# Optimization experiments

Measured on AMD Instinct MI355X. Metric: run time of the kernel, lower is better.

Reference implementation:

```python
import jax, jax.numpy as jnp
import numpy as np

B, L, E, H = 1, 2048, 1024, 16
D = E // H
SCALE_BASE = 512.0
LN_EPS = 1e-5


def _rotate_every_two(x):
    x1 = x[..., ::2]
    x2 = x[..., 1::2]
    return jnp.stack((-x2, x1), axis=-1).reshape(x.shape)


def _xpos(x, downscale):
    # x: [B, H, L, D]; offset=0 path of torchscale XPOS
    length, dim = x.shape[-2], x.shape[-1]
    half = dim // 2
    base_scale = (jnp.arange(0, dim, 2, dtype=jnp.float32) + 0.4 * dim) / (1.4 * dim)  # [half]
    min_pos = -(length // 2)
    pos = jnp.arange(min_pos, min_pos + length, dtype=jnp.float32)  # [L]
    scale = base_scale[None, :] ** (pos[:, None] / SCALE_BASE)  # [L, half]
    inv_freq = 1.0 / (10000.0 ** (jnp.arange(half, dtype=jnp.float32) / half))
    sinusoid = jnp.arange(length, dtype=jnp.float32)[:, None] * inv_freq[None, :]  # [L, half]
    sin, cos = jnp.sin(sinusoid), jnp.cos(sinusoid)
    if downscale:
        scale = 1.0 / scale
    sin_s = jnp.repeat(sin * scale, 2, axis=-1)  # duplicate_interleave -> [L, D]
    cos_s = jnp.repeat(cos * scale, 2, axis=-1)
    return x * cos_s + _rotate_every_two(x) * sin_s


def setup_inputs() -> dict:
    key = jax.random.key(0)
    ks = jax.random.split(key, 8)
    s = 1.0 / np.sqrt(E)
    causal = jnp.where(jnp.triu(jnp.ones((L, L), dtype=bool), 1), -1e9, 0.0).astype(jnp.float32)
    return {
        "query": jax.random.normal(ks[0], (B, L, E), jnp.float32),
        "rel_pos": jax.random.normal(ks[1], (B * H, L, L), jnp.float32) * 0.02,
        "attn_mask": causal,
        "wq": jax.random.normal(ks[2], (E, E), jnp.float32) * s,
        "bq": jnp.zeros((E,), jnp.float32),
        "wk": jax.random.normal(ks[3], (E, E), jnp.float32) * s,
        "bk": jnp.zeros((E,), jnp.float32),
        "wv": jax.random.normal(ks[4], (E, E), jnp.float32) * s,
        "bv": jnp.zeros((E,), jnp.float32),
        "wo": jax.random.normal(ks[5], (E, E), jnp.float32) * s,
        "bo": jnp.zeros((E,), jnp.float32),
        "ln_g": jnp.ones((E,), jnp.float32),
        "ln_b": jnp.zeros((E,), jnp.float32),
    }


def reference(query, rel_pos, attn_mask, wq, bq, wk, bk, wv, bv, wo, bo, ln_g, ln_b):
    b, l, e = query.shape
    # QKV projections (self-attention: key=value=query)
    def split_heads(x):
        return x.reshape(b, l, H, D).transpose(0, 2, 1, 3)  # [B,H,L,D]
    q = split_heads(query @ wq.T + bq)
    k = split_heads(query @ wk.T + bk)
    v = split_heads(query @ wv.T + bv)
    # xpos rotary: keys downscaled, queries upscaled (offset=0, prefill)
    k = _xpos(k, downscale=True)
    q = _xpos(q, downscale=False)
    # scaled dot-product attention with additive causal mask + rel_pos bias
    q = q * (D ** -0.5)
    aw = jnp.einsum("bhtd,bhsd->bhts", q, k)
    aw = aw + attn_mask[None, None, :, :]
    aw = aw + rel_pos.reshape(b, H, l, l)
    aw = jax.nn.softmax(aw.astype(jnp.float32), axis=-1).astype(q.dtype)
    attn = jnp.einsum("bhts,bhsd->bhtd", aw, v)
    attn = attn.transpose(0, 2, 1, 3).reshape(b, l, e)  # [B, L, E]
    # inner_attn_ln (subln)
    mu = jnp.mean(attn, axis=-1, keepdims=True)
    var = jnp.mean((attn - mu) ** 2, axis=-1, keepdims=True)
    attn = (attn - mu) / jnp.sqrt(var + LN_EPS) * ln_g + ln_b
    out = attn @ wo.T + bo
    return out, aw.reshape(b * H, l, l)
```

## Files before the change

### kernel.cpp

```cpp
#include <hip/hip_runtime.h>
#include <cmath>

#define L_SEQ 2048
#define E_DIM 1024
#define NH    16
#define HD    64

typedef float v4f __attribute__((ext_vector_type(4)));


__global__ __launch_bounds__(256) void gemm128(
    const float* __restrict__ A,
    const float* __restrict__ Wq, const float* __restrict__ bq_, float* __restrict__ oq,
    const float* __restrict__ Wk, const float* __restrict__ bk_, float* __restrict__ ok_,
    const float* __restrict__ Wv, const float* __restrict__ bv_, float* __restrict__ ov,
    int mode_in)
{
  __shared__ float As[64][132];
  __shared__ float Ws[64][68];
  const int tid = threadIdx.x;
  const int tx = tid & 15, ty = tid >> 4;
  const int n0 = blockIdx.x * 64;
  const int m0 = blockIdx.y * 128;
  const int mode = (mode_in < 0) ? (int)blockIdx.z : mode_in;
  const float* W    = (mode == 1) ? Wk  : (mode == 2) ? Wv  : Wq;
  const float* bias = (mode == 1) ? bk_ : (mode == 2) ? bv_ : bq_;
  float* outp       = (mode == 1) ? ok_ : (mode == 2) ? ov  : oq;

  float acc[8][4] = {};
  for (int k0 = 0; k0 < E_DIM; k0 += 64) {
#pragma unroll
    for (int jj = 0; jj < 8; ++jj) {
      int idx = jj * 256 + tid;
      int r = idx >> 4, c4 = idx & 15;
      float4 a4 = *(const float4*)&A[(size_t)(m0 + r) * E_DIM + k0 + 4 * c4];
      As[4*c4+0][r] = a4.x; As[4*c4+1][r] = a4.y;
      As[4*c4+2][r] = a4.z; As[4*c4+3][r] = a4.w;
    }
#pragma unroll
    for (int jj = 0; jj < 4; ++jj) {
      int idx = jj * 256 + tid;
      int r = idx >> 4, c4 = idx & 15;
      float4 w4 = *(const float4*)&W[(size_t)(n0 + r) * E_DIM + k0 + 4 * c4];
      Ws[4*c4+0][r] = w4.x; Ws[4*c4+1][r] = w4.y;
      Ws[4*c4+2][r] = w4.z; Ws[4*c4+3][r] = w4.w;
    }
    __syncthreads();
#pragma unroll 16
    for (int kk = 0; kk < 64; ++kk) {
      float4 a0 = *(const float4*)&As[kk][8 * ty];
      float4 a1 = *(const float4*)&As[kk][8 * ty + 4];
      float4 b0 = *(const float4*)&Ws[kk][4 * tx];
      float av[8] = {a0.x, a0.y, a0.z, a0.w, a1.x, a1.y, a1.z, a1.w};
      float bv4[4] = {b0.x, b0.y, b0.z, b0.w};
#pragma unroll
      for (int i = 0; i < 8; ++i)
#pragma unroll
        for (int j = 0; j < 4; ++j) acc[i][j] += av[i] * bv4[j];
    }
    __syncthreads();
  }

  if (mode <= 1) {
    const int h = n0 >> 6;
    const float invf0 = powf(10000.0f, -(float)(2*tx + 0) * (1.0f/32.0f));
    const float invf1 = powf(10000.0f, -(float)(2*tx + 1) * (1.0f/32.0f));
    const float base0 = (2.0f*(2*tx + 0) + 0.4f*HD) / (1.4f*HD);
    const float base1 = (2.0f*(2*tx + 1) + 0.4f*HD) / (1.4f*HD);
#pragma unroll
    for (int i = 0; i < 8; ++i) {
      int t = m0 + 8*ty + i;
      float pe = (float)(t - L_SEQ/2) * (1.0f/512.0f);
#pragma unroll
      for (int jp = 0; jp < 2; ++jp) {
        int j = 2*jp;
        int d = 4*tx + j;
        float x0 = acc[i][j]   + bias[n0 + d];
        float x1 = acc[i][j+1] + bias[n0 + d + 1];
        float sc = powf(jp ? base1 : base0, pe);
        if (mode == 1) sc = 1.0f / sc;
        float invf = jp ? invf1 : invf0;
        float sn, cs;
        sincosf((float)t * invf, &sn, &cs);
        float y0 = (x0*cs - x1*sn) * sc;
        float y1 = (x1*cs + x0*sn) * sc;
        if (mode == 0) { y0 *= 0.125f; y1 *= 0.125f; }
        acc[i][j] = y0; acc[i][j+1] = y1;
      }
    }
#pragma unroll
    for (int i = 0; i < 8; ++i)
#pragma unroll
      for (int j = 0; j < 4; ++j)
        As[4*tx + j][8*ty + i] = acc[i][j];
    __syncthreads();
    const int row = tid >> 2;
    const size_t obase = ((size_t)(h * HD + row)) * L_SEQ + m0;
#pragma unroll
    for (int c4 = 0; c4 < 8; ++c4) {
      int c = (tid & 3) + 4 * c4;
      *(float4*)&outp[obase + 4*c] = *(const float4*)&As[row][4*c];
    }
  } else if (mode == 2) {
    const int h = n0 >> 6;
#pragma unroll
    for (int i = 0; i < 8; ++i) {
      int m = m0 + 8*ty + i;
      float4 r4;
      r4.x = acc[i][0] + bias[n0 + 4*tx + 0];
      r4.y = acc[i][1] + bias[n0 + 4*tx + 1];
      r4.z = acc[i][2] + bias[n0 + 4*tx + 2];
      r4.w = acc[i][3] + bias[n0 + 4*tx + 3];
      *(float4*)&outp[((size_t)h * L_SEQ + m) * HD + 4*tx] = r4;
    }
  } else {
#pragma unroll
    for (int i = 0; i < 8; ++i) {
      int m = m0 + 8*ty + i;
      float4 r4;
      r4.x = acc[i][0] + bias[n0 + 4*tx + 0];
      r4.y = acc[i][1] + bias[n0 + 4*tx + 1];
      r4.z = acc[i][2] + bias[n0 + 4*tx + 2];
      r4.w = acc[i][3] + bias[n0 + 4*tx + 3];
      *(float4*)&outp[(size_t)m * E_DIM + n0 + 4*tx] = r4;
    }
  }
}

__global__ __launch_bounds__(256) void attn_kernel(
    const float* __restrict__ qT, const float* __restrict__ kT,
    const float* __restrict__ v,  const float* __restrict__ rel,
    float* __restrict__ aw, float* __restrict__ attn)
{
  __shared__ float qs[64][68];
  __shared__ float ks[64][68];
  const int tid = threadIdx.x;
  const int tx = tid & 15, ty = tid >> 4;
  const int bid = blockIdx.x;
  const int h = bid & 15;
  const int x = bid >> 4;
  const int t0i = (x < 16) ? (31 - x) : (x - 16);
  const int t0 = t0i * 64;
  const int nt = t0i + 1;

#pragma unroll
  for (int jj = 0; jj < 4; ++jj) {
    int idx = jj * 256 + tid;
    int d = idx >> 4, c = (idx & 15) * 4;
    *(float4*)&qs[d][c] = *(const float4*)&qT[((size_t)(h*HD + d)) * L_SEQ + t0 + c];
  }

  float m_run[4], l_run[4];
#pragma unroll
  for (int i = 0; i < 4; ++i) { m_run[i] = -3.0e38f; l_run[i] = 0.0f; }

  for (int st = 0; st < nt; ++st) {
    const int s0 = st * 64;
#pragma unroll
    for (int jj = 0; jj < 4; ++jj) {
      int idx = jj * 256 + tid;
      int d = idx >> 4, c = (idx & 15) * 4;
      *(float4*)&ks[d][c] = *(const float4*)&kT[((size_t)(h*HD + d)) * L_SEQ + s0 + c];
    }
    __syncthreads();
    float acc[4][4] = {};
#pragma unroll 16
    for (int kk = 0; kk < 64; ++kk) {
      float4 a0 = *(const float4*)&qs[kk][4 * ty];
      float4 b0 = *(const float4*)&ks[kk][4 * tx];
      float av[4] = {a0.x, a0.y, a0.z, a0.w};
      float bv4[4] = {b0.x, b0.y, b0.z, b0.w};
#pragma unroll
      for (int i = 0; i < 4; ++i)
#pragma unroll
        for (int j = 0; j < 4; ++j) acc[i][j] += av[i] * bv4[j];
    }
    const bool diag = (s0 == t0);
#pragma unroll
    for (int i = 0; i < 4; ++i) {
      int t = t0 + 4*ty + i;
      size_t off = ((size_t)(h * L_SEQ + t)) * L_SEQ + s0 + 4*tx;
      if (diag) {
        int sb = s0 + 4*tx;
        if (sb + 0 > t) acc[i][0] += -1.0e9f;
        if (sb + 1 > t) acc[i][1] += -1.0e9f;
        if (sb + 2 > t) acc[i][2] += -1.0e9f;
        if (sb + 3 > t) acc[i][3] += -1.0e9f;
      }
      v4f rp = __builtin_nontemporal_load((const v4f*)(rel + off));
      acc[i][0] += rp.x; acc[i][1] += rp.y; acc[i][2] += rp.z; acc[i][3] += rp.w;
      float4 s4 = {acc[i][0], acc[i][1], acc[i][2], acc[i][3]};
      *(float4*)(aw + off) = s4;
      float rmx = fmaxf(fmaxf(acc[i][0], acc[i][1]), fmaxf(acc[i][2], acc[i][3]));
      rmx = fmaxf(rmx, __shfl_xor(rmx, 1));
      rmx = fmaxf(rmx, __shfl_xor(rmx, 2));
      rmx = fmaxf(rmx, __shfl_xor(rmx, 4));
      rmx = fmaxf(rmx, __shfl_xor(rmx, 8));
      float mnew = fmaxf(m_run[i], rmx);
      float se = __expf(acc[i][0] - mnew) + __expf(acc[i][1] - mnew)
               + __expf(acc[i][2] - mnew) + __expf(acc[i][3] - mnew);
      se += __shfl_xor(se, 1);
      se += __shfl_xor(se, 2);
      se += __shfl_xor(se, 4);
      se += __shfl_xor(se, 8);
      l_run[i] = l_run[i] * __expf(m_run[i] - mnew) + se;
      m_run[i] = mnew;
    }
    __syncthreads();
  }

  float il[4];
#pragma unroll
  for (int i = 0; i < 4; ++i) il[i] = 1.0f / l_run[i];

  float (*ps)[68] = qs;
  float (*vs)[68] = ks;
  float pacc[4][4] = {};
  for (int st = 0; st < nt; ++st) {
    const int s0 = st * 64;
#pragma unroll
    for (int jj = 0; jj < 4; ++jj) {
      int idx = jj * 256 + tid;
      int r = idx >> 4, c = (idx & 15) * 4;
      *(float4*)&vs[r][c] = *(const float4*)&v[((size_t)(h * L_SEQ) + s0 + r) * HD + c];
    }
    float p[4][4];
#pragma unroll
    for (int i = 0; i < 4; ++i) {
      int t = t0 + 4*ty + i;
      size_t off = ((size_t)(h * L_SEQ + t)) * L_SEQ + s0 + 4*tx;
      float4 s4 = *(const float4*)(aw + off);
      p[i][0] = __expf(s4.x - m_run[i]) * il[i];
      p[i][1] = __expf(s4.y - m_run[i]) * il[i];
      p[i][2] = __expf(s4.z - m_run[i]) * il[i];
      p[i][3] = __expf(s4.w - m_run[i]) * il[i];
      v4f o4 = {p[i][0], p[i][1], p[i][2], p[i][3]};
      __builtin_nontemporal_store(o4, (v4f*)(aw + off));
    }
#pragma unroll
    for (int j = 0; j < 4; ++j) {
      float4 col = {p[0][j], p[1][j], p[2][j], p[3][j]};
      *(float4*)&ps[4*tx + j][4*ty] = col;
    }
    __syncthreads();
#pragma unroll 16
    for (int ss = 0; ss < 64; ++ss) {
      float4 a0 = *(const float4*)&ps[ss][4 * ty];
      float4 b0 = *(const float4*)&vs[ss][4 * tx];
      float av[4] = {a0.x, a0.y, a0.z, a0.w};
      float bv4[4] = {b0.x, b0.y, b0.z, b0.w};
#pragma unroll
      for (int i = 0; i < 4; ++i)
#pragma unroll
        for (int j = 0; j < 4; ++j) pacc[i][j] += av[i] * bv4[j];
    }
    __syncthreads();
  }

  const int zs = t0 + 64;
  if (zs < L_SEQ) {
    const v4f z4 = {0.f, 0.f, 0.f, 0.f};
    const int nz4 = (L_SEQ - zs) >> 2;
    for (int r = tid >> 6; r < 64; r += 4) {
      v4f* dst = (v4f*)(aw + ((size_t)(h * L_SEQ + t0 + r)) * L_SEQ + zs);
      for (int c = (tid & 63); c < nz4; c += 64)
        __builtin_nontemporal_store(z4, dst + c);
    }
  }

#pragma unroll
  for (int i = 0; i < 4; ++i) {
    int t = t0 + 4*ty + i;
    float4 r4 = {pacc[i][0], pacc[i][1], pacc[i][2], pacc[i][3]};
    *(float4*)&attn[(size_t)t * E_DIM + h*HD + 4*tx] = r4;
  }
}

__global__ __launch_bounds__(256) void ln_kernel(
    float* __restrict__ attn, const float* __restrict__ g, const float* __restrict__ b)
{
  __shared__ float r1[256], r2[256];
  const int tid = threadIdx.x;
  float* xrow = attn + (size_t)blockIdx.x * E_DIM;
  float4 xv = *(float4*)&xrow[4 * tid];
  float s = xv.x + xv.y + xv.z + xv.w;
  float sq = xv.x*xv.x + xv.y*xv.y + xv.z*xv.z + xv.w*xv.w;
  r1[tid] = s; r2[tid] = sq;
  __syncthreads();
  for (int o = 128; o > 0; o >>= 1) {
    if (tid < o) { r1[tid] += r1[tid + o]; r2[tid] += r2[tid + o]; }
    __syncthreads();
  }
  float mu = r1[0] * (1.0f / E_DIM);
  float var = r2[0] * (1.0f / E_DIM) - mu * mu;
  float inv = rsqrtf(var + 1e-5f);
  float4 gv = *(const float4*)&g[4 * tid];
  float4 bv = *(const float4*)&b[4 * tid];
  float4 ov;
  ov.x = (xv.x - mu) * inv * gv.x + bv.x;
  ov.y = (xv.y - mu) * inv * gv.y + bv.y;
  ov.z = (xv.z - mu) * inv * gv.z + bv.z;
  ov.w = (xv.w - mu) * inv * gv.w + bv.w;
  *(float4*)&xrow[4 * tid] = ov;
}

extern "C" void kernel_launch(void* const* d_in, const int* in_sizes, int n_in,
                              void* d_out, int out_size, void* d_ws, size_t ws_size,
                              hipStream_t stream) {
  const float* query = (const float*)d_in[0];
  const float* rel   = (const float*)d_in[1];
  const float* wq    = (const float*)d_in[3];
  const float* bq    = (const float*)d_in[4];
  const float* wk    = (const float*)d_in[5];
  const float* bk    = (const float*)d_in[6];
  const float* wv    = (const float*)d_in[7];
  const float* bv    = (const float*)d_in[8];
  const float* wo    = (const float*)d_in[9];
  const float* bo    = (const float*)d_in[10];
  const float* ln_g  = (const float*)d_in[11];
  const float* ln_b  = (const float*)d_in[12];

  float* out = (float*)d_out;
  float* aw  = out + (size_t)L_SEQ * E_DIM;

  float* ws   = (float*)d_ws;
  float* qT   = ws;
  float* kT   = ws + 1 * 2097152;
  float* vb   = ws + 2 * 2097152;
  float* attn = ws + 3 * 2097152;

  dim3 blk(256);
  gemm128<<<dim3(16, 16, 3), blk, 0, stream>>>(query,
      wq, bq, qT, wk, bk, kT, wv, bv, vb, -1);
  attn_kernel<<<dim3(512), blk, 0, stream>>>(qT, kT, vb, rel, aw, attn);
  ln_kernel<<<dim3(L_SEQ), blk, 0, stream>>>(attn, ln_g, ln_b);
  gemm128<<<dim3(16, 16, 1), blk, 0, stream>>>(attn,
      wo, bo, out, wo, bo, out, wo, bo, out, 3);
}
```

Before: 1.069 ms.

## Register-prefetch GEMM and attention tiles, halve attention query tile to 32 rows

The GEMM now prefetches the next K-slice of A and W into registers while computing on the current shared-memory tile. The attention kernel uses 32-row query tiles and launches 1024 blocks, which doubles parallelism and reduces wasted causal work. It also prefetches K, V and the stored scores into registers one tile ahead so global loads overlap with compute. In exchange, K/V traffic per query row goes up, the register-held prefetch raises register pressure, and arithmetic intensity per thread is lower.

```diff
diff --git a/kernel.cpp b/kernel.cpp
--- a/kernel.cpp
+++ b/kernel.cpp
@@ -27,25 +27,35 @@
   const float* bias = (mode == 1) ? bk_ : (mode == 2) ? bv_ : bq_;
   float* outp       = (mode == 1) ? ok_ : (mode == 2) ? ov  : oq;
 
+  const float* ap = A + (size_t)(m0 + ty) * E_DIM + 4 * tx;
+  const float* wp = W + (size_t)(n0 + ty) * E_DIM + 4 * tx;
+
+  float4 pa[8], pw[4];
+#pragma unroll
+  for (int jj = 0; jj < 8; ++jj) pa[jj] = *(const float4*)&ap[(size_t)jj * 16 * E_DIM];
+#pragma unroll
+  for (int jj = 0; jj < 4; ++jj) pw[jj] = *(const float4*)&wp[(size_t)jj * 16 * E_DIM];
+
   float acc[8][4] = {};
   for (int k0 = 0; k0 < E_DIM; k0 += 64) {
+    __syncthreads();
 #pragma unroll
     for (int jj = 0; jj < 8; ++jj) {
-      int idx = jj * 256 + tid;
-      int r = idx >> 4, c4 = idx & 15;
-      float4 a4 = *(const float4*)&A[(size_t)(m0 + r) * E_DIM + k0 + 4 * c4];
-      As[4*c4+0][r] = a4.x; As[4*c4+1][r] = a4.y;
-      As[4*c4+2][r] = a4.z; As[4*c4+3][r] = a4.w;
+      As[4*tx+0][jj*16+ty] = pa[jj].x; As[4*tx+1][jj*16+ty] = pa[jj].y;
+      As[4*tx+2][jj*16+ty] = pa[jj].z; As[4*tx+3][jj*16+ty] = pa[jj].w;
     }
 #pragma unroll
     for (int jj = 0; jj < 4; ++jj) {
-      int idx = jj * 256 + tid;
-      int r = idx >> 4, c4 = idx & 15;
-      float4 w4 = *(const float4*)&W[(size_t)(n0 + r) * E_DIM + k0 + 4 * c4];
-      Ws[4*c4+0][r] = w4.x; Ws[4*c4+1][r] = w4.y;
-      Ws[4*c4+2][r] = w4.z; Ws[4*c4+3][r] = w4.w;
-    }
-    __syncthreads();
+      Ws[4*tx+0][jj*16+ty] = pw[jj].x; Ws[4*tx+1][jj*16+ty] = pw[jj].y;
+      Ws[4*tx+2][jj*16+ty] = pw[jj].z; Ws[4*tx+3][jj*16+ty] = pw[jj].w;
+    }
+    __syncthreads();
+    if (k0 + 64 < E_DIM) {
+#pragma unroll
+      for (int jj = 0; jj < 8; ++jj) pa[jj] = *(const float4*)&ap[(size_t)jj*16*E_DIM + k0 + 64];
+#pragma unroll
+      for (int jj = 0; jj < 4; ++jj) pw[jj] = *(const float4*)&wp[(size_t)jj*16*E_DIM + k0 + 64];
+    }
 #pragma unroll 16
     for (int kk = 0; kk < 64; ++kk) {
       float4 a0 = *(const float4*)&As[kk][8 * ty];
@@ -58,8 +68,8 @@
 #pragma unroll
         for (int j = 0; j < 4; ++j) acc[i][j] += av[i] * bv4[j];
     }
-    __syncthreads();
-  }
+  }
+  __syncthreads();
 
   if (mode <= 1) {
     const int h = n0 >> 6;
@@ -132,147 +142,172 @@
     const float* __restrict__ v,  const float* __restrict__ rel,
     float* __restrict__ aw, float* __restrict__ attn)
 {
-  __shared__ float qs[64][68];
+  __shared__ float qs[64][36];
   __shared__ float ks[64][68];
   const int tid = threadIdx.x;
   const int tx = tid & 15, ty = tid >> 4;
   const int bid = blockIdx.x;
   const int h = bid & 15;
-  const int x = bid >> 4;
-  const int t0i = (x < 16) ? (31 - x) : (x - 16);
-  const int t0 = t0i * 64;
-  const int nt = t0i + 1;
-
-#pragma unroll
-  for (int jj = 0; jj < 4; ++jj) {
+  const int ti = 63 - (bid >> 4);
+  const int t0 = ti * 32;
+  const int nt = ((t0 + 31) >> 6) + 1;
+
+#pragma unroll
+  for (int jj = 0; jj < 2; ++jj) {
     int idx = jj * 256 + tid;
-    int d = idx >> 4, c = (idx & 15) * 4;
+    int d = idx >> 3, c = (idx & 7) * 4;
     *(float4*)&qs[d][c] = *(const float4*)&qT[((size_t)(h*HD + d)) * L_SEQ + t0 + c];
   }
 
-  float m_run[4], l_run[4];
-#pragma unroll
-  for (int i = 0; i < 4; ++i) { m_run[i] = -3.0e38f; l_run[i] = 0.0f; }
+  const float* kbase = kT + (size_t)(h*HD + ty) * L_SEQ + 4*tx;
+  const size_t row0 = (size_t)(h * L_SEQ + t0 + 2*ty) * L_SEQ + 4*tx;
+  const size_t row1 = row0 + L_SEQ;
+
+  float4 kr[4];
+#pragma unroll
+  for (int jj = 0; jj < 4; ++jj) kr[jj] = *(const float4*)&kbase[(size_t)jj*16*L_SEQ];
+
+  float m_run[2] = {-3.0e38f, -3.0e38f};
+  float l_run[2] = {0.0f, 0.0f};
 
   for (int st = 0; st < nt; ++st) {
     const int s0 = st * 64;
-#pragma unroll
-    for (int jj = 0; jj < 4; ++jj) {
-      int idx = jj * 256 + tid;
-      int d = idx >> 4, c = (idx & 15) * 4;
-      *(float4*)&ks[d][c] = *(const float4*)&kT[((size_t)(h*HD + d)) * L_SEQ + s0 + c];
-    }
-    __syncthreads();
-    float acc[4][4] = {};
+    __syncthreads();
+#pragma unroll
+    for (int jj = 0; jj < 4; ++jj)
+      *(float4*)&ks[jj*16 + ty][4*tx] = kr[jj];
+    __syncthreads();
+    if (st + 1 < nt) {
+#pragma unroll
+      for (int jj = 0; jj < 4; ++jj)
+        kr[jj] = *(const float4*)&kbase[(size_t)jj*16*L_SEQ + s0 + 64];
+    }
+    float4 rp0 = *(const float4*)&rel[row0 + s0];
+    float4 rp1 = *(const float4*)&rel[row1 + s0];
+
+    float acc[2][4] = {};
 #pragma unroll 16
     for (int kk = 0; kk < 64; ++kk) {
-      float4 a0 = *(const float4*)&qs[kk][4 * ty];
+      float2 a0 = *(const float2*)&qs[kk][2 * ty];
       float4 b0 = *(const float4*)&ks[kk][4 * tx];
-      float av[4] = {a0.x, a0.y, a0.z, a0.w};
       float bv4[4] = {b0.x, b0.y, b0.z, b0.w};
 #pragma unroll
-      for (int i = 0; i < 4; ++i)
-#pragma unroll
-        for (int j = 0; j < 4; ++j) acc[i][j] += av[i] * bv4[j];
-    }
-    const bool diag = (s0 == t0);
-#pragma unroll
-    for (int i = 0; i < 4; ++i) {
-      int t = t0 + 4*ty + i;
-      size_t off = ((size_t)(h * L_SEQ + t)) * L_SEQ + s0 + 4*tx;
-      if (diag) {
-        int sb = s0 + 4*tx;
-        if (sb + 0 > t) acc[i][0] += -1.0e9f;
-        if (sb + 1 > t) acc[i][1] += -1.0e9f;
-        if (sb + 2 > t) acc[i][2] += -1.0e9f;
-        if (sb + 3 > t) acc[i][3] += -1.0e9f;
+      for (int j = 0; j < 4; ++j) {
+        acc[0][j] += a0.x * bv4[j];
+        acc[1][j] += a0.y * bv4[j];
       }
-      v4f rp = __builtin_nontemporal_load((const v4f*)(rel + off));
-      acc[i][0] += rp.x; acc[i][1] += rp.y; acc[i][2] += rp.z; acc[i][3] += rp.w;
-      float4 s4 = {acc[i][0], acc[i][1], acc[i][2], acc[i][3]};
-      *(float4*)(aw + off) = s4;
-      float rmx = fmaxf(fmaxf(acc[i][0], acc[i][1]), fmaxf(acc[i][2], acc[i][3]));
+    }
+    if (st == nt - 1) {
+      int sb = s0 + 4*tx;
+#pragma unroll
+      for (int r = 0; r < 2; ++r) {
+        int t = t0 + 2*ty + r;
+#pragma unroll
+        for (int j = 0; j < 4; ++j)
+          if (sb + j > t) acc[r][j] += -1.0e9f;
+      }
+    }
+    acc[0][0] += rp0.x; acc[0][1] += rp0.y; acc[0][2] += rp0.z; acc[0][3] += rp0.w;
+    acc[1][0] += rp1.x; acc[1][1] += rp1.y; acc[1][2] += rp1.z; acc[1][3] += rp1.w;
+    {
+      float4 s4 = {acc[0][0], acc[0][1], acc[0][2], acc[0][3]};
+      *(float4*)(aw + row0 + s0) = s4;
+      float4 s5 = {acc[1][0], acc[1][1], acc[1][2], acc[1][3]};
+      *(float4*)(aw + row1 + s0) = s5;
+    }
+#pragma unroll
+    for (int r = 0; r < 2; ++r) {
+      float rmx = fmaxf(fmaxf(acc[r][0], acc[r][1]), fmaxf(acc[r][2], acc[r][3]));
       rmx = fmaxf(rmx, __shfl_xor(rmx, 1));
       rmx = fmaxf(rmx, __shfl_xor(rmx, 2));
       rmx = fmaxf(rmx, __shfl_xor(rmx, 4));
       rmx = fmaxf(rmx, __shfl_xor(rmx, 8));
-      float mnew = fmaxf(m_run[i], rmx);
-      float se = __expf(acc[i][0] - mnew) + __expf(acc[i][1] - mnew)
-               + __expf(acc[i][2] - mnew) + __expf(acc[i][3] - mnew);
+      float mnew = fmaxf(m_run[r], rmx);
+      float se = __expf(acc[r][0] - mnew) + __expf(acc[r][1] - mnew)
+               + __expf(acc[r][2] - mnew) + __expf(acc[r][3] - mnew);
       se += __shfl_xor(se, 1);
       se += __shfl_xor(se, 2);
       se += __shfl_xor(se, 4);
       se += __shfl_xor(se, 8);
-      l_run[i] = l_run[i] * __expf(m_run[i] - mnew) + se;
-      m_run[i] = mnew;
-    }
-    __syncthreads();
-  }
-
-  float il[4];
-#pragma unroll
-  for (int i = 0; i < 4; ++i) il[i] = 1.0f / l_run[i];
-
-  float (*ps)[68] = qs;
+      l_run[r] = l_run[r] * __expf(m_run[r] - mnew) + se;
+      m_run[r] = mnew;
+    }
+  }
+
+  const float il0 = 1.0f / l_run[0], il1 = 1.0f / l_run[1];
+  float (*ps)[36] = qs;
   float (*vs)[68] = ks;
-  float pacc[4][4] = {};
+  const float* vbase = v + ((size_t)(h * L_SEQ) + ty) * HD + 4*tx;
+
+  float4 sv0 = *(const float4*)(aw + row0);
+  float4 sv1 = *(const float4*)(aw + row1);
+  float4 vr[4];
+#pragma unroll
+  for (int jj = 0; jj < 4; ++jj) vr[jj] = *(const float4*)&vbase[(size_t)jj*16*HD];
+
+  float pacc[2][4] = {};
   for (int st = 0; st < nt; ++st) {
     const int s0 = st * 64;
-#pragma unroll
-    for (int jj = 0; jj < 4; ++jj) {
-      int idx = jj * 256 + tid;
-      int r = idx >> 4, c = (idx & 15) * 4;
-      *(float4*)&vs[r][c] = *(const float4*)&v[((size_t)(h * L_SEQ) + s0 + r) * HD + c];
-    }
-    float p[4][4];
-#pragma unroll
-    for (int i = 0; i < 4; ++i) {
-      int t = t0 + 4*ty + i;
-      size_t off = ((size_t)(h * L_SEQ + t)) * L_SEQ + s0 + 4*tx;
-      float4 s4 = *(const float4*)(aw + off);
-      p[i][0] = __expf(s4.x - m_run[i]) * il[i];
-      p[i][1] = __expf(s4.y - m_run[i]) * il[i];
-      p[i][2] = __expf(s4.z - m_run[i]) * il[i];
-      p[i][3] = __expf(s4.w - m_run[i]) * il[i];
-      v4f o4 = {p[i][0], p[i][1], p[i][2], p[i][3]};
-      __builtin_nontemporal_store(o4, (v4f*)(aw + off));
-    }
+    float p0[4], p1[4];
+    p0[0] = __expf(sv0.x - m_run[0]) * il0;
+    p0[1] = __expf(sv0.y - m_run[0]) * il0;
+    p0[2] = __expf(sv0.z - m_run[0]) * il0;
+    p0[3] = __expf(sv0.w - m_run[0]) * il0;
+    p1[0] = __expf(sv1.x - m_run[1]) * il1;
+    p1[1] = __expf(sv1.y - m_run[1]) * il1;
+    p1[2] = __expf(sv1.z - m_run[1]) * il1;
+    p1[3] = __expf(sv1.w - m_run[1]) * il1;
+    {
+      v4f o0 = {p0[0], p0[1], p0[2], p0[3]};
+      __builtin_nontemporal_store(o0, (v4f*)(aw + row0 + s0));
+      v4f o1 = {p1[0], p1[1], p1[2], p1[3]};
+      __builtin_nontemporal_store(o1, (v4f*)(aw + row1 + s0));
+    }
+    __syncthreads();
+#pragma unroll
+    for (int jj = 0; jj < 4; ++jj)
+      *(float4*)&vs[jj*16 + ty][4*tx] = vr[jj];
 #pragma unroll
     for (int j = 0; j < 4; ++j) {
-      float4 col = {p[0][j], p[1][j], p[2][j], p[3][j]};
-      *(float4*)&ps[4*tx + j][4*ty] = col;
-    }
-    __syncthreads();
+      float2 col = {p0[j], p1[j]};
+      *(float2*)&ps[4*tx + j][2*ty] = col;
+    }
+    __syncthreads();
+    if (st + 1 < nt) {
+      sv0 = *(const float4*)(aw + row0 + s0 + 64);
+      sv1 = *(const float4*)(aw + row1 + s0 + 64);
+#pragma unroll
+      for (int jj = 0; jj < 4; ++jj)
+        vr[jj] = *(const float4*)&vbase[(size_t)(s0 + 64 + jj*16)*HD];
+    }
 #pragma unroll 16
     for (int ss = 0; ss < 64; ++ss) {
-      float4 a0 = *(const float4*)&ps[ss][4 * ty];
+      float2 a0 = *(const float2*)&ps[ss][2 * ty];
       float4 b0 = *(const float4*)&vs[ss][4 * tx];
-      float av[4] = {a0.x, a0.y, a0.z, a0.w};
       float bv4[4] = {b0.x, b0.y, b0.z, b0.w};
 #pragma unroll
-      for (int i = 0; i < 4; ++i)
-#pragma unroll
-        for (int j = 0; j < 4; ++j) pacc[i][j] += av[i] * bv4[j];
-    }
-    __syncthreads();
-  }
-
-  const int zs = t0 + 64;
+      for (int j = 0; j < 4; ++j) {
+        pacc[0][j] += a0.x * bv4[j];
+        pacc[1][j] += a0.y * bv4[j];
+      }
+    }
+  }
+
+  const int zs = 64 * nt;
   if (zs < L_SEQ) {
     const v4f z4 = {0.f, 0.f, 0.f, 0.f};
     const int nz4 = (L_SEQ - zs) >> 2;
-    for (int r = tid >> 6; r < 64; r += 4) {
-      v4f* dst = (v4f*)(aw + ((size_t)(h * L_SEQ + t0 + r)) * L_SEQ + zs);
-      for (int c = (tid & 63); c < nz4; c += 64)
-        __builtin_nontemporal_store(z4, dst + c);
-    }
-  }
-
-#pragma unroll
-  for (int i = 0; i < 4; ++i) {
-    int t = t0 + 4*ty + i;
-    float4 r4 = {pacc[i][0], pacc[i][1], pacc[i][2], pacc[i][3]};
-    *(float4*)&attn[(size_t)t * E_DIM + h*HD + 4*tx] = r4;
+    const int r = tid >> 3;
+    v4f* dst = (v4f*)(aw + ((size_t)(h * L_SEQ + t0 + r)) * L_SEQ + zs);
+    for (int c = (tid & 7); c < nz4; c += 8)
+      __builtin_nontemporal_store(z4, dst + c);
+  }
+
+  {
+    float4 r4 = {pacc[0][0], pacc[0][1], pacc[0][2], pacc[0][3]};
+    *(float4*)&attn[(size_t)(t0 + 2*ty) * E_DIM + h*HD + 4*tx] = r4;
+    float4 r5 = {pacc[1][0], pacc[1][1], pacc[1][2], pacc[1][3]};
+    *(float4*)&attn[(size_t)(t0 + 2*ty + 1) * E_DIM + h*HD + 4*tx] = r5;
   }
 }
 
@@ -332,7 +367,7 @@
   dim3 blk(256);
   gemm128<<<dim3(16, 16, 3), blk, 0, stream>>>(query,
       wq, bq, qT, wk, bk, kT, wv, bv, vb, -1);
-  attn_kernel<<<dim3(512), blk, 0, stream>>>(qT, kT, vb, rel, aw, attn);
+  attn_kernel<<<dim3(1024), blk, 0, stream>>>(qT, kT, vb, rel, aw, attn);
   ln_kernel<<<dim3(L_SEQ), blk, 0, stream>>>(attn, ln_g, ln_b);
   gemm128<<<dim3(16, 16, 1), blk, 0, stream>>>(attn,
       wo, bo, out, wo, bo, out, wo, bo, out, 3);
```

Measured after the change: 1.060 ms. About the same (-0.9%).
